# Kernel optimization log

Measured on AMD Instinct MI355X. Metric: run time of the kernel, lower is better.

Reference implementation:

```python
import jax, jax.numpy as jnp
import numpy as np

B, L, H, E = 4, 2048, 8, 64
S, D = L, E

def setup_inputs() -> dict:
    key = jax.random.key(0)
    kq, kk, kv = jax.random.split(key, 3)
    queries = jax.random.normal(kq, (B, L, H, E), dtype=jnp.float32)
    keys = jax.random.normal(kk, (B, S, H, E), dtype=jnp.float32)
    values = jax.random.normal(kv, (B, S, H, D), dtype=jnp.float32)
    # TriangularCausalMask: True above the diagonal -> masked out
    attn_mask = jnp.broadcast_to(
        jnp.triu(jnp.ones((L, S), dtype=bool), k=1)[None, None], (B, 1, L, S)
    )
    return {"queries": queries, "keys": keys, "values": values, "attn_mask": attn_mask}

def reference(queries, keys, values, attn_mask):
    E_ = queries.shape[-1]
    scale = 1.0 / jnp.sqrt(jnp.float32(E_))
    # scores: [B, H, L, S]
    scores = jnp.einsum('blhe,bshe->bhls', queries, keys)
    scores = jnp.where(attn_mask, -jnp.inf, scores)
    A = jax.nn.softmax(scale * scores, axis=-1)  # dropout p=0.01 omitted (eval/deterministic)
    V = jnp.einsum('bhls,bshd->blhd', A, values)
    return (V, A)
```

## Files before the change

### kernel.cpp

```cpp
#include <hip/hip_runtime.h>
#include <hip/hip_bf16.h>
#include <stdint.h>
#include <stddef.h>

typedef __bf16 bf16;
typedef __attribute__((ext_vector_type(8))) __bf16 bf16x8;
typedef __attribute__((ext_vector_type(4))) float f32x4;
typedef unsigned short u16;
typedef __attribute__((ext_vector_type(4))) u16 u16x4;

#define NB 4
#define NL 2048
#define NH 8
#define NE 64
#define NS 2048
#define ND 64
#define CM 0.18033688011112042f
#define STR 72

__device__ __forceinline__ void barrier_keep_vm() {
    asm volatile("s_waitcnt lgkmcnt(0)" ::: "memory");
    __builtin_amdgcn_s_barrier();
    asm volatile("" ::: "memory");
}

__global__ __launch_bounds__(512, 4)
void attn_fwd(const float* __restrict__ Qg, const float* __restrict__ Kg,
              const float* __restrict__ Vg, float* __restrict__ Og,
              float* __restrict__ Ag)
{
    __shared__ __attribute__((aligned(16))) bf16 Kl[2][64 * STR];
    __shared__ __attribute__((aligned(16))) bf16 Vl[2][64 * STR];
    __shared__ __attribute__((aligned(16))) bf16 Pl[8][16 * STR];

    const int bid = blockIdx.x;
    const int x   = bid & 7;
    const int u   = bid >> 3;
    const int qb  = (u < 32) ? (u & 15) : 15 - (u & 15);
    const int bh  = x * 4 + (u >> 4);
    const int b   = bh >> 3;
    const int h   = bh & 7;
    const int q0  = qb * 128;
    const int jmax = 2 * qb + 1;

    const int tid  = threadIdx.x;
    const int wid  = tid >> 6;
    const int lane = tid & 63;
    const int g    = lane >> 4;
    const int li   = lane & 15;
    const int jd   = 2 * qb + (wid >> 2);

    const float* qp = Qg + (((size_t)b * NL + q0 + wid * 16 + li) * NH + h) * NE;
    bf16x8 qf[2];
#pragma unroll
    for (int t = 0; t < 2; ++t) {
        f32x4 x0 = *(const f32x4*)(qp + t * 32 + g * 8);
        f32x4 x1 = *(const f32x4*)(qp + t * 32 + g * 8 + 4);
        bf16x8 v;
#pragma unroll
        for (int e = 0; e < 4; ++e) { v[e] = (bf16)x0[e]; v[4 + e] = (bf16)x1[e]; }
        qf[t] = v;
    }

    float* Abase = Ag + (((size_t)(b * NH + h)) * NL + q0) * NS;

    const int srow = tid >> 3;
    const int scb  = (tid & 7) * 8;
    const float* kbase = Kg + (((size_t)b * NS + srow) * NH + h) * NE + scb;
    const float* vbase = Vg + (((size_t)b * NS + srow) * NH + h) * ND + scb;

    auto loadK = [&](int j, f32x4 r[2]) {
        const float* src = kbase + (size_t)j * 64 * NH * NE;
        r[0] = *(const f32x4*)(src);
        r[1] = *(const f32x4*)(src + 4);
    };
    auto loadV = [&](int j, f32x4 r[2]) {
        const float* src = vbase + (size_t)j * 64 * NH * ND;
        r[0] = *(const f32x4*)(src);
        r[1] = *(const f32x4*)(src + 4);
    };
    auto writeK = [&](int c, const f32x4 r[2]) {
        bf16x8 w;
#pragma unroll
        for (int e = 0; e < 4; ++e) { w[e] = (bf16)r[0][e]; w[4 + e] = (bf16)r[1][e]; }
        *(bf16x8*)(Kl[c] + srow * STR + scb) = w;
    };
    auto writeV = [&](int c, const f32x4 r[2]) {
#pragma unroll
        for (int e = 0; e < 8; ++e) {
            int d    = scb + e;
            int boff = (srow * 2) ^ (d & 48);
            *(bf16*)((char*)Vl[c] + (size_t)d * (2 * STR) + boff) = (bf16)r[e >> 2][e & 3];
        }
    };

    auto computeScores = [&](int c, int j, float sv[4][4]) {
        const bf16* kl = Kl[c];
#pragma unroll
        for (int ct = 0; ct < 4; ++ct) {
            f32x4 a = {0.f, 0.f, 0.f, 0.f};
#pragma unroll
            for (int t = 0; t < 2; ++t) {
                bf16x8 kb = *(const bf16x8*)(kl + (size_t)(ct * 16 + li) * STR + 32 * t + 8 * g);
                a = __builtin_amdgcn_mfma_f32_16x16x32_bf16(qf[t], kb, a, 0, 0, 0);
            }
            if (j == jd) {
#pragma unroll
                for (int r = 0; r < 4; ++r) {
                    int scol = j * 64 + ct * 16 + li;
                    int qrow = q0 + wid * 16 + g * 4 + r;
                    sv[ct][r] = (scol > qrow) ? -1e30f : a[r] * CM;
                }
            } else {
#pragma unroll
                for (int r = 0; r < 4; ++r) sv[ct][r] = a[r] * CM;
            }
        }
    };

    f32x4 kr[2], vr[2];
    loadK(0, kr);
    float psum[4] = {0.f, 0.f, 0.f, 0.f};
    for (int j = 0; j <= jmax; ++j) {
        const int c = j & 1;
        writeK(c, kr);
        if (j < jmax) loadK(j + 1, kr);
        barrier_keep_vm();
        if (j <= jd) {
            float sv[4][4];
            computeScores(c, j, sv);
#pragma unroll
            for (int r = 0; r < 4; ++r) {
                float s0 = __builtin_amdgcn_exp2f(sv[0][r]) + __builtin_amdgcn_exp2f(sv[1][r]);
                float s1 = __builtin_amdgcn_exp2f(sv[2][r]) + __builtin_amdgcn_exp2f(sv[3][r]);
                psum[r] += s0 + s1;
            }
        }
    }

    loadK(0, kr);
    loadV(0, vr);

    float vinv[4];
#pragma unroll
    for (int r = 0; r < 4; ++r) {
        float s = psum[r];
#pragma unroll
        for (int mk = 1; mk < 16; mk <<= 1) s += __shfl_xor(s, mk);
        vinv[r] = 1.f / s;
    }

    f32x4 oacc[4];
#pragma unroll
    for (int dt = 0; dt < 4; ++dt) oacc[dt] = (f32x4){0.f, 0.f, 0.f, 0.f};

    barrier_keep_vm();

    for (int j = 0; j < 32; ++j) {
        const int c = j & 1;
        if (j <= jmax) {
            writeK(c, kr);
            writeV(c, vr);
            if (j < jmax) { loadK(j + 1, kr); loadV(j + 1, vr); }
            barrier_keep_vm();
        }

        float* arow = Abase + (size_t)(wid * 16) * NS + j * 64;

        if (j <= jd) {
            float sv[4][4];
            computeScores(c, j, sv);

            bf16* pl = &Pl[wid][0];
#pragma unroll
            for (int ct = 0; ct < 4; ++ct)
#pragma unroll
                for (int r = 0; r < 4; ++r) {
                    float p = __builtin_amdgcn_exp2f(sv[ct][r]) * vinv[r];
                    pl[(size_t)(g * 4 + r) * STR + ct * 16 + li] = (bf16)p;
                }
            asm volatile("s_waitcnt lgkmcnt(0)" ::: "memory");
            __builtin_amdgcn_sched_barrier(0);

#pragma unroll
            for (int s = 0; s < 4; ++s) {
                int row = g + s * 4;
                u16x4 pw = *(const u16x4*)(pl + (size_t)row * STR + li * 4);
                f32x4 o;
#pragma unroll
                for (int e = 0; e < 4; ++e) {
                    uint32_t w = ((uint32_t)pw[e]) << 16;
                    o[e] = __builtin_bit_cast(float, w);
                }
                __builtin_nontemporal_store(o, (f32x4*)(arow + (size_t)row * NS + li * 4));
            }

#pragma unroll
            for (int t = 0; t < 2; ++t) {
                bf16x8 pa = *(const bf16x8*)(pl + (size_t)li * STR + 32 * t + 8 * g);
#pragma unroll
                for (int dt = 0; dt < 4; ++dt) {
                    bf16x8 vb = *(const bf16x8*)((const char*)Vl[c]
                                  + (size_t)(dt * 16 + li) * (2 * STR)
                                  + ((64 * t + 16 * g) ^ (dt * 16 & 48)));
                    oacc[dt] = __builtin_amdgcn_mfma_f32_16x16x32_bf16(pa, vb, oacc[dt], 0, 0, 0);
                }
            }
        } else {
            f32x4 z = {0.f, 0.f, 0.f, 0.f};
#pragma unroll
            for (int s = 0; s < 4; ++s) {
                int row = g + s * 4;
                __builtin_nontemporal_store(z, (f32x4*)(arow + (size_t)row * NS + li * 4));
            }
        }
    }

#pragma unroll
    for (int dt = 0; dt < 4; ++dt)
#pragma unroll
        for (int r = 0; r < 4; ++r) {
            float* op = Og + (((size_t)b * NL + q0 + wid * 16 + g * 4 + r) * NH + h) * ND
                        + dt * 16 + li;
            __builtin_nontemporal_store(oacc[dt][r], op);
        }
}

extern "C" void kernel_launch(void* const* d_in, const int* in_sizes, int n_in,
                              void* d_out, int out_size, void* d_ws, size_t ws_size,
                              hipStream_t stream) {
    (void)in_sizes; (void)n_in; (void)out_size; (void)d_ws; (void)ws_size;
    const float* Q = (const float*)d_in[0];
    const float* K = (const float*)d_in[1];
    const float* V = (const float*)d_in[2];
    float* out = (float*)d_out;
    float* Og  = out;
    float* Ag  = out + (size_t)NB * NL * NH * ND;

    attn_fwd<<<dim3(512), dim3(512), 0, stream>>>(Q, K, V, Og, Ag);
}
```

Before: 147.2 us.

## Pair complementary causal query tiles per block and spread zero-fill of masked scores

Each block now handles two 64-row query tiles, qb and 31-qb, so every block does a balanced amount of causal work instead of relying on a 128-row tile ordering. The zero writes to the masked upper triangle of A are spread across warps that are idle in both passes, with any leftover units written after the loop. The output O is staged through shared memory so it can be written with 16-byte stores. The cost is extra bookkeeping for the zero-fill schedule and a barrier before the output staging.

```diff
diff --git a/kernel.cpp b/kernel.cpp
--- a/kernel.cpp
+++ b/kernel.cpp
@@ -17,6 +17,7 @@
 #define ND 64
 #define CM 0.18033688011112042f
 #define STR 72
+#define KBUFB (64 * STR * 2)
 
 __device__ __forceinline__ void barrier_keep_vm() {
     asm volatile("s_waitcnt lgkmcnt(0)" ::: "memory");
@@ -29,28 +30,26 @@
               const float* __restrict__ Vg, float* __restrict__ Og,
               float* __restrict__ Ag)
 {
-    __shared__ __attribute__((aligned(16))) bf16 Kl[2][64 * STR];
-    __shared__ __attribute__((aligned(16))) bf16 Vl[2][64 * STR];
-    __shared__ __attribute__((aligned(16))) bf16 Pl[8][16 * STR];
+    __shared__ __attribute__((aligned(16))) char smem[6 * KBUFB];
 
     const int bid = blockIdx.x;
     const int x   = bid & 7;
     const int u   = bid >> 3;
-    const int qb  = (u < 32) ? (u & 15) : 15 - (u & 15);
+    const int qb  = u & 15;
     const int bh  = x * 4 + (u >> 4);
     const int b   = bh >> 3;
     const int h   = bh & 7;
-    const int q0  = qb * 128;
-    const int jmax = 2 * qb + 1;
+    const int JH  = 31 - qb;
 
     const int tid  = threadIdx.x;
     const int wid  = tid >> 6;
     const int lane = tid & 63;
     const int g    = lane >> 4;
     const int li   = lane & 15;
-    const int jd   = 2 * qb + (wid >> 2);
-
-    const float* qp = Qg + (((size_t)b * NL + q0 + wid * 16 + li) * NH + h) * NE;
+    const int jd   = (wid < 4) ? qb : JH;
+    const int qrow0 = jd * 64 + (wid & 3) * 16;
+
+    const float* qp = Qg + (((size_t)b * NL + qrow0 + li) * NH + h) * NE;
     bf16x8 qf[2];
 #pragma unroll
     for (int t = 0; t < 2; ++t) {
@@ -62,7 +61,29 @@
         qf[t] = v;
     }
 
-    float* Abase = Ag + (((size_t)(b * NH + h)) * NL + q0) * NS;
+    float* Ahead = Ag + (size_t)bh * NL * NS;
+
+    int zc = 0;
+    auto zbase = [&](int unit, int& base, int& col) {
+        if (unit < qb) { base = JH * 64; col = 31 - unit; }
+        else           { base = qb * 64; col = 31 - (unit - qb); }
+    };
+    auto zunit256 = [&](int unit) {
+        int base, col; zbase(unit, base, col);
+        float* p = Ahead + (size_t)(base + (tid >> 2)) * NS + col * 64 + (tid & 3) * 16;
+        f32x4 z = {0.f, 0.f, 0.f, 0.f};
+        __builtin_nontemporal_store(z, (f32x4*)p);
+        __builtin_nontemporal_store(z, (f32x4*)(p + 4));
+        __builtin_nontemporal_store(z, (f32x4*)(p + 8));
+        __builtin_nontemporal_store(z, (f32x4*)(p + 12));
+    };
+    auto zunit512 = [&](int unit) {
+        int base, col; zbase(unit, base, col);
+        float* p = Ahead + (size_t)(base + (tid >> 3)) * NS + col * 64 + (tid & 7) * 8;
+        f32x4 z = {0.f, 0.f, 0.f, 0.f};
+        __builtin_nontemporal_store(z, (f32x4*)p);
+        __builtin_nontemporal_store(z, (f32x4*)(p + 4));
+    };
 
     const int srow = tid >> 3;
     const int scb  = (tid & 7) * 8;
@@ -79,23 +100,22 @@
         r[0] = *(const f32x4*)(src);
         r[1] = *(const f32x4*)(src + 4);
     };
-    auto writeK = [&](int c, const f32x4 r[2]) {
+    auto writeK = [&](char* buf, const f32x4 r[2]) {
         bf16x8 w;
 #pragma unroll
         for (int e = 0; e < 4; ++e) { w[e] = (bf16)r[0][e]; w[4 + e] = (bf16)r[1][e]; }
-        *(bf16x8*)(Kl[c] + srow * STR + scb) = w;
-    };
-    auto writeV = [&](int c, const f32x4 r[2]) {
+        *(bf16x8*)((bf16*)buf + srow * STR + scb) = w;
+    };
+    auto writeV = [&](char* buf, const f32x4 r[2]) {
 #pragma unroll
         for (int e = 0; e < 8; ++e) {
             int d    = scb + e;
             int boff = (srow * 2) ^ (d & 48);
-            *(bf16*)((char*)Vl[c] + (size_t)d * (2 * STR) + boff) = (bf16)r[e >> 2][e & 3];
-        }
-    };
-
-    auto computeScores = [&](int c, int j, float sv[4][4]) {
-        const bf16* kl = Kl[c];
+            *(bf16*)(buf + (size_t)d * (2 * STR) + boff) = (bf16)r[e >> 2][e & 3];
+        }
+    };
+    auto computeScores = [&](const char* buf, int j, float sv[4][4]) {
+        const bf16* kl = (const bf16*)buf;
 #pragma unroll
         for (int ct = 0; ct < 4; ++ct) {
             f32x4 a = {0.f, 0.f, 0.f, 0.f};
@@ -108,7 +128,7 @@
 #pragma unroll
                 for (int r = 0; r < 4; ++r) {
                     int scol = j * 64 + ct * 16 + li;
-                    int qrow = q0 + wid * 16 + g * 4 + r;
+                    int qrow = qrow0 + g * 4 + r;
                     sv[ct][r] = (scol > qrow) ? -1e30f : a[r] * CM;
                 }
             } else {
@@ -121,26 +141,29 @@
     f32x4 kr[2], vr[2];
     loadK(0, kr);
     float psum[4] = {0.f, 0.f, 0.f, 0.f};
-    for (int j = 0; j <= jmax; ++j) {
-        const int c = j & 1;
-        writeK(c, kr);
-        if (j < jmax) loadK(j + 1, kr);
+    for (int j = 0; j <= JH; ++j) {
+        char* kb = smem + (j & 1) * KBUFB;
+        writeK(kb, kr);
+        if (j < JH) loadK(j + 1, kr);
         barrier_keep_vm();
         if (j <= jd) {
             float sv[4][4];
-            computeScores(c, j, sv);
+            computeScores(kb, j, sv);
 #pragma unroll
             for (int r = 0; r < 4; ++r) {
                 float s0 = __builtin_amdgcn_exp2f(sv[0][r]) + __builtin_amdgcn_exp2f(sv[1][r]);
                 float s1 = __builtin_amdgcn_exp2f(sv[2][r]) + __builtin_amdgcn_exp2f(sv[3][r]);
                 psum[r] += s0 + s1;
             }
-        }
+        } else if (tid < 256) {
+            if (zc < 31) zunit256(zc);
+            if (zc + 1 < 31) zunit256(zc + 1);
+        }
+        if (j > qb) zc = (zc + 2 < 31) ? zc + 2 : 31;
     }
 
     loadK(0, kr);
     loadV(0, vr);
-
     float vinv[4];
 #pragma unroll
     for (int r = 0; r < 4; ++r) {
@@ -154,24 +177,21 @@
 #pragma unroll
     for (int dt = 0; dt < 4; ++dt) oacc[dt] = (f32x4){0.f, 0.f, 0.f, 0.f};
 
+    bf16* pl = (bf16*)(smem + 4 * KBUFB) + wid * 16 * STR;
+
     barrier_keep_vm();
 
-    for (int j = 0; j < 32; ++j) {
-        const int c = j & 1;
-        if (j <= jmax) {
-            writeK(c, kr);
-            writeV(c, vr);
-            if (j < jmax) { loadK(j + 1, kr); loadV(j + 1, vr); }
-            barrier_keep_vm();
-        }
-
-        float* arow = Abase + (size_t)(wid * 16) * NS + j * 64;
+    for (int j = 0; j <= JH; ++j) {
+        char* kb   = smem + (j & 1) * KBUFB;
+        char* vbuf = smem + (2 + (j & 1)) * KBUFB;
+        writeK(kb, kr);
+        writeV(vbuf, vr);
+        if (j < JH) { loadK(j + 1, kr); loadV(j + 1, vr); }
+        barrier_keep_vm();
 
         if (j <= jd) {
             float sv[4][4];
-            computeScores(c, j, sv);
-
-            bf16* pl = &Pl[wid][0];
+            computeScores(kb, j, sv);
 #pragma unroll
             for (int ct = 0; ct < 4; ++ct)
 #pragma unroll
@@ -182,6 +202,7 @@
             asm volatile("s_waitcnt lgkmcnt(0)" ::: "memory");
             __builtin_amdgcn_sched_barrier(0);
 
+            float* arow = Ahead + (size_t)qrow0 * NS + j * 64;
 #pragma unroll
             for (int s = 0; s < 4; ++s) {
                 int row = g + s * 4;
@@ -194,36 +215,42 @@
                 }
                 __builtin_nontemporal_store(o, (f32x4*)(arow + (size_t)row * NS + li * 4));
             }
-
 #pragma unroll
             for (int t = 0; t < 2; ++t) {
                 bf16x8 pa = *(const bf16x8*)(pl + (size_t)li * STR + 32 * t + 8 * g);
 #pragma unroll
                 for (int dt = 0; dt < 4; ++dt) {
-                    bf16x8 vb = *(const bf16x8*)((const char*)Vl[c]
+                    bf16x8 vb = *(const bf16x8*)(vbuf
                                   + (size_t)(dt * 16 + li) * (2 * STR)
                                   + ((64 * t + 16 * g) ^ (dt * 16 & 48)));
                     oacc[dt] = __builtin_amdgcn_mfma_f32_16x16x32_bf16(pa, vb, oacc[dt], 0, 0, 0);
                 }
             }
-        } else {
-            f32x4 z = {0.f, 0.f, 0.f, 0.f};
-#pragma unroll
-            for (int s = 0; s < 4; ++s) {
-                int row = g + s * 4;
-                __builtin_nontemporal_store(z, (f32x4*)(arow + (size_t)row * NS + li * 4));
-            }
-        }
-    }
-
+        } else if (tid < 256) {
+            if (zc < 31) zunit256(zc);
+            if (zc + 1 < 31) zunit256(zc + 1);
+        }
+        if (j > qb) zc = (zc + 2 < 31) ? zc + 2 : 31;
+    }
+
+    for (; zc < 31; ++zc) zunit512(zc);
+
+    barrier_keep_vm();
+    float* scr = (float*)smem + wid * 1024;
 #pragma unroll
     for (int dt = 0; dt < 4; ++dt)
 #pragma unroll
-        for (int r = 0; r < 4; ++r) {
-            float* op = Og + (((size_t)b * NL + q0 + wid * 16 + g * 4 + r) * NH + h) * ND
-                        + dt * 16 + li;
-            __builtin_nontemporal_store(oacc[dt][r], op);
-        }
+        for (int r = 0; r < 4; ++r)
+            scr[(g * 4 + r) * 64 + dt * 16 + li] = oacc[dt][r];
+    asm volatile("s_waitcnt lgkmcnt(0)" ::: "memory");
+    __builtin_amdgcn_sched_barrier(0);
+#pragma unroll
+    for (int s = 0; s < 4; ++s) {
+        int row = g + s * 4;
+        f32x4 o = *(const f32x4*)(scr + row * 64 + li * 4);
+        float* op = Og + (((size_t)b * NL + qrow0 + row) * NH + h) * ND + li * 4;
+        __builtin_nontemporal_store(o, (f32x4*)op);
+    }
 }
 
 extern "C" void kernel_launch(void* const* d_in, const int* in_sizes, int n_in,
```

Result: slower. 444.2 us (+201.8%).
